# Kernel optimization log

Hardware: AMD Instinct MI355X
Metric: run time of the kernel (lower is better)

Reference implementation:

```python
import jax, jax.numpy as jnp
import numpy as np

NUM_HEADS = 4
LN_EPS = 1e-5


def setup_inputs() -> dict:
    key = jax.random.key(0)
    ks = jax.random.split(key, 12)
    B, S, D = 8, 2048, 256
    Dh = D // NUM_HEADS
    s = 0.02
    return {
        "descriptors": jax.random.normal(ks[0], (B, S, D), jnp.float32),
        # cached rotary embedding (cos, sin) pair broadcastable over heads
        "keypoints": jax.random.normal(ks[1], (2, B, 1, S, Dh), jnp.float32),
        "Wqkv_w": jax.random.normal(ks[2], (3 * D, D), jnp.float32) * s,
        "Wqkv_b": jax.random.normal(ks[3], (3 * D,), jnp.float32) * s,
        "Wo_w": jax.random.normal(ks[4], (D, D), jnp.float32) * s,
        "Wo_b": jax.random.normal(ks[5], (D,), jnp.float32) * s,
        "W1_w": jax.random.normal(ks[6], (2 * D, 2 * D), jnp.float32) * s,
        "W1_b": jax.random.normal(ks[7], (2 * D,), jnp.float32) * s,
        "ln_g": jnp.ones((2 * D,), jnp.float32),
        "ln_b": jnp.zeros((2 * D,), jnp.float32),
        "W2_w": jax.random.normal(ks[8], (D, 2 * D), jnp.float32) * s,
        "W2_b": jax.random.normal(ks[9], (D,), jnp.float32) * s,
    }


def _rotate_half(x):
    # pairwise rotation: (x0,x1,x2,x3,...) -> (-x1,x0,-x3,x2,...)
    xr = x.reshape(x.shape[:-1] + (x.shape[-1] // 2, 2))
    return jnp.stack((-xr[..., 1], xr[..., 0]), axis=-1).reshape(x.shape)


def reference(descriptors, keypoints, Wqkv_w, Wqkv_b, Wo_w, Wo_b,
              W1_w, W1_b, ln_g, ln_b, W2_w, W2_b):
    B, S, D = descriptors.shape
    H = NUM_HEADS
    Dh = D // H
    # fused QKV projection; torch layout: last dim = (H, Dh, 3) interleaved
    qkv = descriptors @ Wqkv_w.T + Wqkv_b           # [B,S,3D]
    qkv = qkv.reshape(B, S, H, Dh, 3).transpose(0, 2, 1, 3, 4)  # [B,H,S,Dh,3]
    q, k, v = qkv[..., 0], qkv[..., 1], qkv[..., 2]
    # rotary embedding on q, k
    cos, sin = keypoints[0], keypoints[1]           # [B,1,S,Dh]
    q = q * cos + _rotate_half(q) * sin
    k = k * cos + _rotate_half(k) * sin
    # scaled dot-product attention
    scale = jnp.float32(Dh) ** -0.5
    sim = jnp.einsum('bhid,bhjd->bhij', q, k) * scale
    attn = jax.nn.softmax(sim, axis=-1)
    ctx = jnp.einsum('bhij,bhjd->bhid', attn, v)    # [B,H,S,Dh]
    ctx = ctx.transpose(0, 2, 1, 3).reshape(B, S, D)
    message = ctx @ Wo_w.T + Wo_b
    # FFN over concat(descriptors, message)
    x = jnp.concatenate([descriptors, message], axis=-1)  # [B,S,2D]
    x = x @ W1_w.T + W1_b
    mu = jnp.mean(x, axis=-1, keepdims=True)
    var = jnp.var(x, axis=-1, keepdims=True)
    x = (x - mu) * jax.lax.rsqrt(var + LN_EPS) * ln_g + ln_b
    x = jax.nn.gelu(x, approximate=False)
    x = x @ W2_w.T + W2_b
    return descriptors + x
```

## Files before the change

kernel.cpp:

```cpp
#include <hip/hip_runtime.h>
#include <math.h>

#define B_  8
#define S_  2048
#define D_  256
#define H_  4
#define DH  64
#define M_  (B_ * S_)
#define QS  4194304

typedef __attribute__((ext_vector_type(8))) short bf16x8;
typedef __attribute__((ext_vector_type(4))) float f32x4;
typedef unsigned short u16;
typedef unsigned int   u32;

#define AS1 __attribute__((address_space(1)))
#define AS3 __attribute__((address_space(3)))

__device__ __forceinline__ u16 f2bf(float x) {
    union { float f; u32 u; } c; c.f = x;
    u32 r = (c.u + 0x7fffu + ((c.u >> 16) & 1u)) >> 16;
    return (u16)r;
}
__device__ __forceinline__ float bf2f(u16 x) {
    union { u32 u; float f; } c; c.u = ((u32)x) << 16;
    return c.f;
}

__device__ __forceinline__ void gload16(const void* g, void* l) {
    __builtin_amdgcn_global_load_lds((const AS1 unsigned int*)g,
                                     (AS3 unsigned int*)l, 16, 0, 0);
}

__global__ __launch_bounds__(256) void cast5_kernel(
    const float* __restrict__ s0, u16* __restrict__ d0,
    const float* __restrict__ s1, u16* __restrict__ d1,
    const float* __restrict__ s2, u16* __restrict__ d2,
    const float* __restrict__ s3, u16* __restrict__ d3,
    const float* __restrict__ s4, u16* __restrict__ d4)
{
    int bid = blockIdx.x;
    const float* s; u16* d;
    if      (bid < 4096) { s = s0; d = d0; }
    else if (bid < 4288) { s = s1; d = d1; bid -= 4096; }
    else if (bid < 4352) { s = s2; d = d2; bid -= 4288; }
    else if (bid < 4608) { s = s3; d = d3; bid -= 4352; }
    else                 { s = s4; d = d4; bid -= 4608; }
    const int i = (bid * 256 + threadIdx.x) * 4;
    const float4 v = *(const float4*)(s + i);
    u16 o[4] = {f2bf(v.x), f2bf(v.y), f2bf(v.z), f2bf(v.w)};
    *(uint2*)(d + i) = *(const uint2*)o;
}

template <int NT, int CONCAT, int RES, int OUTBF16>
__global__ __launch_bounds__(256) void gemm_bf16(
    const u16* __restrict__ A, const u16* __restrict__ A2,
    const u16* __restrict__ W, const float* __restrict__ bias,
    const float* __restrict__ res, float* __restrict__ Cf,
    u16* __restrict__ Cb, int K, int N)
{
    __shared__ u16 As[128 * 64];
    __shared__ u16 Bs[NT * 32 * 64];
    const int tid  = threadIdx.x;
    const int w    = tid >> 6;
    const int lane = tid & 63;
    const int n    = lane & 15;
    const int quad = lane >> 4;
    const int m0   = blockIdx.x * 128;
    const int n0   = blockIdx.y * (NT * 32);
    const int m_off = (w >> 1) * 64;
    const int n_off = (w & 1) * (NT * 16);
    const int lrow = lane >> 3;
    const int lcol = (lane & 7) * 8;

    f32x4 acc[4][NT];
#pragma unroll
    for (int i = 0; i < 4; i++)
#pragma unroll
        for (int j = 0; j < NT; j++) acc[i][j] = (f32x4){0.f, 0.f, 0.f, 0.f};

    for (int k0 = 0; k0 < K; k0 += 64) {
        const u16* Asrc;
        int kb, lda;
        if (CONCAT) { Asrc = (k0 < 256) ? A : A2; kb = k0 & 255; lda = 256; }
        else        { Asrc = A; kb = k0; lda = K; }

        __syncthreads();
#pragma unroll
        for (int it = 0; it < 4; it++) {
            const int r0 = it * 32 + w * 8;
            gload16(Asrc + (size_t)(m0 + r0 + lrow) * lda + kb + lcol, &As[r0 * 64]);
        }
#pragma unroll
        for (int it = 0; it < NT; it++) {
            const int r0 = it * 32 + w * 8;
            gload16(W + (size_t)(n0 + r0 + lrow) * K + k0 + lcol, &Bs[r0 * 64]);
        }
        __syncthreads();

        bf16x8 af[4][2], bf[NT][2];
#pragma unroll
        for (int mt = 0; mt < 4; mt++)
#pragma unroll
            for (int t = 0; t < 2; t++)
                af[mt][t] = *(const bf16x8*)&As[(m_off + mt * 16 + n) * 64 + t * 32 + quad * 8];
#pragma unroll
        for (int nt = 0; nt < NT; nt++)
#pragma unroll
            for (int t = 0; t < 2; t++)
                bf[nt][t] = *(const bf16x8*)&Bs[(n_off + nt * 16 + n) * 64 + t * 32 + quad * 8];

#pragma unroll
        for (int mt = 0; mt < 4; mt++)
#pragma unroll
            for (int nt = 0; nt < NT; nt++) {
                acc[mt][nt] = __builtin_amdgcn_mfma_f32_16x16x32_bf16(af[mt][0], bf[nt][0], acc[mt][nt], 0, 0, 0);
                acc[mt][nt] = __builtin_amdgcn_mfma_f32_16x16x32_bf16(af[mt][1], bf[nt][1], acc[mt][nt], 0, 0, 0);
            }
    }

#pragma unroll
    for (int nt = 0; nt < NT; nt++) {
        const int col = n0 + n_off + nt * 16 + n;
        const float bv = bias[col];
#pragma unroll
        for (int mt = 0; mt < 4; mt++) {
#pragma unroll
            for (int r = 0; r < 4; r++) {
                const int row = m0 + m_off + mt * 16 + quad * 4 + r;
                float o = acc[mt][nt][r] + bv;
                if (RES) o += res[(size_t)row * N + col];
                if (OUTBF16) Cb[(size_t)row * N + col] = f2bf(o);
                else         Cf[(size_t)row * N + col] = o;
            }
        }
    }
}

__global__ __launch_bounds__(256) void rope_kernel(
    const u16* __restrict__ qkv, const float* __restrict__ kp,
    u16* __restrict__ q, u16* __restrict__ k, u16* __restrict__ v)
{
    const int row = blockIdx.x * 2 + (threadIdx.x >> 7);
    const int t   = threadIdx.x & 127;
    const int b   = row >> 11;
    const int s   = row & 2047;
    const int h   = t >> 5;
    const int dp  = t & 31;
    const int d   = dp * 2;

    const u16* src = qkv + (size_t)row * 768 + h * 192 + dp * 6;
    const u32 w0 = *(const u32*)(src);
    const u32 w1 = *(const u32*)(src + 2);
    const u32 w2 = *(const u32*)(src + 4);
    const float qe = bf2f((u16)w0), ke = bf2f((u16)(w0 >> 16));
    const float qo = bf2f((u16)(w1 >> 16));
    const float ko = bf2f((u16)w2);

    const size_t kidx = ((size_t)b * S_ + s) * DH + d;
    const float2 cs = *(const float2*)(kp + kidx);
    const float2 sn = *(const float2*)(kp + (size_t)B_ * S_ * DH + kidx);

    const float qe2 = (qe * cs.x - qo * sn.x) * 0.125f;
    const float qo2 = (qo * cs.y + qe * sn.y) * 0.125f;
    const float ke2 = ke * cs.x - ko * sn.x;
    const float ko2 = ko * cs.y + ke * sn.y;

    const size_t oidx = (((size_t)(b * H_ + h)) * S_ + s) * DH + d;
    *(u32*)(q + oidx) = (u32)f2bf(qe2) | ((u32)f2bf(qo2) << 16);
    *(u32*)(k + oidx) = (u32)f2bf(ke2) | ((u32)f2bf(ko2) << 16);
    *(u32*)(v + oidx) = (w1 & 0xffffu) | (w2 & 0xffff0000u);
}

__global__ __launch_bounds__(256) void vtrans_kernel(
    const u16* __restrict__ v, u16* __restrict__ vt)
{
    const int bh = blockIdx.x;
    const int s  = blockIdx.y * 256 + threadIdx.x;
    const u16* src = v + ((size_t)bh * S_ + s) * DH;
    u16* dst = vt + (size_t)bh * DH * S_ + s;
#pragma unroll
    for (int g = 0; g < 8; g++) {
        const uint4 vv = *(const uint4*)(src + g * 8);
        const u16* us = (const u16*)&vv;
#pragma unroll
        for (int i = 0; i < 8; i++) dst[(size_t)(g * 8 + i) * S_] = us[i];
    }
}

__global__ __launch_bounds__(256, 4) void attn_kernel(
    const u16* __restrict__ q, const u16* __restrict__ k,
    const u16* __restrict__ vt, u16* __restrict__ ctx)
{
    __shared__ u16 ks[128 * 64];
    __shared__ u16 vs[64 * 128];
    __shared__ u16 qs[64 * 64];

    const int tid  = threadIdx.x;
    const int w    = tid >> 6;
    const int lane = tid & 63;
    const int n    = lane & 15;
    const int quad = lane >> 4;
    const int lrow = lane >> 3;
    const int vrow = lane >> 4;
    const int bh   = blockIdx.x;
    const int q0   = blockIdx.y * 64;
    const int b    = bh >> 2;
    const int h    = bh & 3;
    const int nsw  = n & 7;

    const int kcol  = (((lane & 7) ^ lrow) * 8);
    const int vcol0 = (((lane & 15) ^ vrow) * 8);
    const int vcol1 = (((lane & 15) ^ (4 + vrow)) * 8);

    const u16* qbase = q  + (size_t)bh * S_ * DH;
    const u16* kbase = k  + (size_t)bh * S_ * DH;
    const u16* vbase = vt + (size_t)bh * DH * S_;

#pragma unroll
    for (int it = 0; it < 2; it++) {
        const int idx = it * 256 + tid;
        const int row = idx >> 3;
        const int c8  = idx & 7;
        *(uint4*)&qs[row * 64 + ((c8 ^ (row & 7)) * 8)] =
            *(const uint4*)(qbase + (size_t)(q0 + row) * DH + c8 * 8);
    }
    __syncthreads();

    bf16x8 qf[2];
    qf[0] = *(const bf16x8*)&qs[(16 * w + n) * 64 + ((quad       ^ nsw) * 8)];
    qf[1] = *(const bf16x8*)&qs[(16 * w + n) * 64 + (((4 + quad) ^ nsw) * 8)];

    f32x4 o[4];
#pragma unroll
    for (int j = 0; j < 4; j++) o[j] = (f32x4){0.f, 0.f, 0.f, 0.f};
    float lrun[4] = {0.f, 0.f, 0.f, 0.f};

    for (int kb = 0; kb < S_ / 128; kb++) {
        const int k0 = kb * 128;
        __syncthreads();
#pragma unroll
        for (int it = 0; it < 4; it++) {
            const int r0 = w * 32 + it * 8;
            gload16(kbase + (size_t)(k0 + r0 + lrow) * DH + kcol, &ks[r0 * 64]);
            const int d0 = w * 16 + it * 4;
            gload16(vbase + (size_t)(d0 + vrow) * S_ + k0 + ((it & 1) ? vcol1 : vcol0),
                    &vs[d0 * 128]);
        }
        __syncthreads();

        f32x4 sacc[8];
#pragma unroll
        for (int j = 0; j < 8; j++)
            sacc[j] = (f32x4){-12.f, -12.f, -12.f, -12.f};
#pragma unroll
        for (int t = 0; t < 2; t++) {
#pragma unroll
            for (int j = 0; j < 8; j++) {
                const bf16x8 kf = *(const bf16x8*)
                    &ks[(16 * j + n) * 64 + (((t * 4 + quad) ^ nsw) * 8)];
                sacc[j] = __builtin_amdgcn_mfma_f32_16x16x32_bf16(qf[t], kf, sacc[j], 0, 0, 0);
            }
        }
        __syncthreads();

#pragma unroll
        for (int r = 0; r < 4; r++) {
            float rs = 0.f;
            const int rw8  = (quad * 4 + r) & 7;
            const int prow = (16 * w + quad * 4 + r) * 128;
#pragma unroll
            for (int j = 0; j < 8; j++) {
                const float p = __expf(sacc[j][r]);
                rs += p;
                ks[prow + (((2 * j + (n >> 3)) ^ rw8) * 8) + (n & 7)] = f2bf(p);
            }
            lrun[r] += rs;
        }

#pragma unroll
        for (int kt = 0; kt < 4; kt++) {
            const bf16x8 pf = *(const bf16x8*)
                &ks[(16 * w + n) * 128 + (((kt * 4 + quad) ^ nsw) * 8)];
#pragma unroll
            for (int nt = 0; nt < 4; nt++) {
                const bf16x8 vf = *(const bf16x8*)
                    &vs[(16 * nt + n) * 128 + (((kt * 4 + quad) ^ nsw) * 8)];
                o[nt] = __builtin_amdgcn_mfma_f32_16x16x32_bf16(pf, vf, o[nt], 0, 0, 0);
            }
        }
    }

#pragma unroll
    for (int r = 0; r < 4; r++) {
        float s = lrun[r];
        s += __shfl_xor(s, 1);
        s += __shfl_xor(s, 2);
        s += __shfl_xor(s, 4);
        s += __shfl_xor(s, 8);
        lrun[r] = s;
    }

#pragma unroll
    for (int r = 0; r < 4; r++) {
        const float inv = 1.f / lrun[r];
        const int row = q0 + 16 * w + quad * 4 + r;
#pragma unroll
        for (int nt = 0; nt < 4; nt++)
            ctx[((size_t)b * S_ + row) * D_ + h * DH + 16 * nt + n] = f2bf(o[nt][r] * inv);
    }
}

__global__ __launch_bounds__(256) void ln_gelu_kernel(
    const float* __restrict__ x, const float* __restrict__ g,
    const float* __restrict__ bt, u16* __restrict__ y)
{
    __shared__ float ss[4], sqs[4];
    const int m = blockIdx.x;
    const float* row = x + (size_t)m * 512;
    const int t = threadIdx.x;
    const float v0 = row[t];
    const float v1 = row[t + 256];
    float s  = v0 + v1;
    float sq = v0 * v0 + v1 * v1;
#pragma unroll
    for (int off = 1; off < 64; off <<= 1) {
        s  += __shfl_xor(s, off);
        sq += __shfl_xor(sq, off);
    }
    const int w = t >> 6;
    if ((t & 63) == 0) { ss[w] = s; sqs[w] = sq; }
    __syncthreads();
    s  = ss[0] + ss[1] + ss[2] + ss[3];
    sq = sqs[0] + sqs[1] + sqs[2] + sqs[3];
    const float mu   = s * (1.f / 512.f);
    const float var  = sq * (1.f / 512.f) - mu * mu;
    const float rstd = rsqrtf(var + 1e-5f);

    const float y0 = (v0 - mu) * rstd * g[t] + bt[t];
    const float y1 = (v1 - mu) * rstd * g[t + 256] + bt[t + 256];
    y[(size_t)m * 512 + t]       = f2bf(0.5f * y0 * (1.f + erff(y0 * 0.70710678118654752f)));
    y[(size_t)m * 512 + t + 256] = f2bf(0.5f * y1 * (1.f + erff(y1 * 0.70710678118654752f)));
}

extern "C" void kernel_launch(void* const* d_in, const int* in_sizes, int n_in,
                              void* d_out, int out_size, void* d_ws, size_t ws_size,
                              hipStream_t stream)
{
    const float* desc   = (const float*)d_in[0];
    const float* kp     = (const float*)d_in[1];
    const float* Wqkv_w = (const float*)d_in[2];
    const float* Wqkv_b = (const float*)d_in[3];
    const float* Wo_w   = (const float*)d_in[4];
    const float* Wo_b   = (const float*)d_in[5];
    const float* W1_w   = (const float*)d_in[6];
    const float* W1_b   = (const float*)d_in[7];
    const float* ln_g   = (const float*)d_in[8];
    const float* ln_b   = (const float*)d_in[9];
    const float* W2_w   = (const float*)d_in[10];
    const float* W2_b   = (const float*)d_in[11];
    float* out = (float*)d_out;
    float* ws  = (float*)d_ws;

    u16*   qkvb  = (u16*)ws;
    float* x1    = ws;
    u16*   x1b   = (u16*)(ws + 2 * (size_t)QS);
    u16*   qb    = (u16*)(ws + 3 * (size_t)QS);
    u16*   kb    = (u16*)(ws + (size_t)(3.5 * QS));
    u16*   vb    = (u16*)(ws + 4 * (size_t)QS);
    u16*   ctxb  = (u16*)(ws + (size_t)(4.5 * QS));
    u16*   descb = (u16*)(ws + 5 * (size_t)QS);
    u16*   msgb  = (u16*)(ws + (size_t)(5.5 * QS));
    u16*   wpool = (u16*)(ws + 6 * (size_t)QS);
    u16*   vtb   = (u16*)(ws + (size_t)(6.5 * QS));
    u16* wqkvb = wpool;
    u16* wob   = wqkvb + 196608;
    u16* w1b   = wob   + 65536;
    u16* w2b   = w1b   + 262144;

    const dim3 blk(256);

    cast5_kernel<<<dim3(4736), blk, 0, stream>>>(
        desc, descb, Wqkv_w, wqkvb, Wo_w, wob, W1_w, w1b, W2_w, w2b);

    gemm_bf16<4, 0, 0, 1><<<dim3(M_ / 128, 768 / 128), blk, 0, stream>>>(
        descb, nullptr, wqkvb, Wqkv_b, nullptr, nullptr, qkvb, 256, 768);

    rope_kernel<<<dim3(M_ / 2), blk, 0, stream>>>(qkvb, kp, qb, kb, vb);

    vtrans_kernel<<<dim3(B_ * H_, S_ / 256), blk, 0, stream>>>(vb, vtb);

    attn_kernel<<<dim3(B_ * H_, S_ / 64), blk, 0, stream>>>(qb, kb, vtb, ctxb);

    gemm_bf16<2, 0, 0, 1><<<dim3(M_ / 128, 256 / 64), blk, 0, stream>>>(
        ctxb, nullptr, wob, Wo_b, nullptr, nullptr, msgb, 256, 256);

    gemm_bf16<4, 1, 0, 0><<<dim3(M_ / 128, 512 / 128), blk, 0, stream>>>(
        descb, msgb, w1b, W1_b, nullptr, x1, nullptr, 512, 512);

    ln_gelu_kernel<<<dim3(M_), blk, 0, stream>>>(x1, ln_g, ln_b, x1b);

    gemm_bf16<2, 0, 1, 0><<<dim3(M_ / 128, 256 / 64), blk, 0, stream>>>(
        x1b, nullptr, w2b, W2_b, desc, out, nullptr, 512, 256);
}
```

Baseline: 258.4 us.

## Process 128 query rows per attention block to reuse K/V tiles

Each attention workgroup now handles 128 query rows (two 16-row sub-tiles per wave) instead of 64, so every K and V tile loaded into shared memory feeds twice as many MFMAs. The shared-memory buffers are merged into one pool, with the P tile written over the K and Q region. This halves the global K/V traffic and the number of tile-load barriers per query row. In exchange it doubles accumulator registers, drops occupancy from 4 to 2 blocks, and halves the grid to 512 blocks.

```diff
diff --git a/kernel.cpp b/kernel.cpp
--- a/kernel.cpp
+++ b/kernel.cpp
@@ -188,13 +188,14 @@
     }
 }
 
-__global__ __launch_bounds__(256, 4) void attn_kernel(
+__global__ __launch_bounds__(256, 2) void attn_kernel(
     const u16* __restrict__ q, const u16* __restrict__ k,
     const u16* __restrict__ vt, u16* __restrict__ ctx)
 {
-    __shared__ u16 ks[128 * 64];
-    __shared__ u16 vs[64 * 128];
-    __shared__ u16 qs[64 * 64];
+    __shared__ u16 pool[3 * 8192];
+    u16* ks = pool;
+    u16* qs = pool + 8192;
+    u16* vs = pool + 16384;
 
     const int tid  = threadIdx.x;
     const int w    = tid >> 6;
@@ -204,7 +205,7 @@
     const int lrow = lane >> 3;
     const int vrow = lane >> 4;
     const int bh   = blockIdx.x;
-    const int q0   = blockIdx.y * 64;
+    const int q0   = blockIdx.y * 128;
     const int b    = bh >> 2;
     const int h    = bh & 3;
     const int nsw  = n & 7;
@@ -218,7 +219,7 @@
     const u16* vbase = vt + (size_t)bh * DH * S_;
 
 #pragma unroll
-    for (int it = 0; it < 2; it++) {
+    for (int it = 0; it < 4; it++) {
         const int idx = it * 256 + tid;
         const int row = idx >> 3;
         const int c8  = idx & 7;
@@ -227,14 +228,19 @@
     }
     __syncthreads();
 
-    bf16x8 qf[2];
-    qf[0] = *(const bf16x8*)&qs[(16 * w + n) * 64 + ((quad       ^ nsw) * 8)];
-    qf[1] = *(const bf16x8*)&qs[(16 * w + n) * 64 + (((4 + quad) ^ nsw) * 8)];
-
-    f32x4 o[4];
-#pragma unroll
-    for (int j = 0; j < 4; j++) o[j] = (f32x4){0.f, 0.f, 0.f, 0.f};
-    float lrun[4] = {0.f, 0.f, 0.f, 0.f};
+    bf16x8 qf[2][2];
+#pragma unroll
+    for (int mb = 0; mb < 2; mb++) {
+        qf[mb][0] = *(const bf16x8*)&qs[(w * 32 + mb * 16 + n) * 64 + ((quad       ^ nsw) * 8)];
+        qf[mb][1] = *(const bf16x8*)&qs[(w * 32 + mb * 16 + n) * 64 + (((4 + quad) ^ nsw) * 8)];
+    }
+
+    f32x4 o[2][4];
+#pragma unroll
+    for (int mb = 0; mb < 2; mb++)
+#pragma unroll
+        for (int j = 0; j < 4; j++) o[mb][j] = (f32x4){0.f, 0.f, 0.f, 0.f};
+    float lrun[2][4] = {{0.f, 0.f, 0.f, 0.f}, {0.f, 0.f, 0.f, 0.f}};
 
     for (int kb = 0; kb < S_ / 128; kb++) {
         const int k0 = kb * 128;
@@ -249,65 +255,80 @@
         }
         __syncthreads();
 
-        f32x4 sacc[8];
-#pragma unroll
-        for (int j = 0; j < 8; j++)
-            sacc[j] = (f32x4){-12.f, -12.f, -12.f, -12.f};
+        f32x4 sacc[2][8];
+#pragma unroll
+        for (int mb = 0; mb < 2; mb++)
+#pragma unroll
+            for (int j = 0; j < 8; j++)
+                sacc[mb][j] = (f32x4){-12.f, -12.f, -12.f, -12.f};
 #pragma unroll
         for (int t = 0; t < 2; t++) {
 #pragma unroll
             for (int j = 0; j < 8; j++) {
                 const bf16x8 kf = *(const bf16x8*)
                     &ks[(16 * j + n) * 64 + (((t * 4 + quad) ^ nsw) * 8)];
-                sacc[j] = __builtin_amdgcn_mfma_f32_16x16x32_bf16(qf[t], kf, sacc[j], 0, 0, 0);
+                sacc[0][j] = __builtin_amdgcn_mfma_f32_16x16x32_bf16(qf[0][t], kf, sacc[0][j], 0, 0, 0);
+                sacc[1][j] = __builtin_amdgcn_mfma_f32_16x16x32_bf16(qf[1][t], kf, sacc[1][j], 0, 0, 0);
             }
         }
         __syncthreads();
 
 #pragma unroll
-        for (int r = 0; r < 4; r++) {
-            float rs = 0.f;
-            const int rw8  = (quad * 4 + r) & 7;
-            const int prow = (16 * w + quad * 4 + r) * 128;
-#pragma unroll
-            for (int j = 0; j < 8; j++) {
-                const float p = __expf(sacc[j][r]);
-                rs += p;
-                ks[prow + (((2 * j + (n >> 3)) ^ rw8) * 8) + (n & 7)] = f2bf(p);
+        for (int mb = 0; mb < 2; mb++) {
+#pragma unroll
+            for (int r = 0; r < 4; r++) {
+                float rs = 0.f;
+                const int rw8  = (quad * 4 + r) & 7;
+                const int prow = (w * 32 + mb * 16 + quad * 4 + r) * 128;
+#pragma unroll
+                for (int j = 0; j < 8; j++) {
+                    const float p = __expf(sacc[mb][j][r]);
+                    rs += p;
+                    pool[prow + (((2 * j + (n >> 3)) ^ rw8) * 8) + (n & 7)] = f2bf(p);
+                }
+                lrun[mb][r] += rs;
             }
-            lrun[r] += rs;
         }
 
 #pragma unroll
         for (int kt = 0; kt < 4; kt++) {
-            const bf16x8 pf = *(const bf16x8*)
-                &ks[(16 * w + n) * 128 + (((kt * 4 + quad) ^ nsw) * 8)];
+            const bf16x8 pf0 = *(const bf16x8*)
+                &pool[(w * 32 +      n) * 128 + (((kt * 4 + quad) ^ nsw) * 8)];
+            const bf16x8 pf1 = *(const bf16x8*)
+                &pool[(w * 32 + 16 + n) * 128 + (((kt * 4 + quad) ^ nsw) * 8)];
 #pragma unroll
             for (int nt = 0; nt < 4; nt++) {
                 const bf16x8 vf = *(const bf16x8*)
                     &vs[(16 * nt + n) * 128 + (((kt * 4 + quad) ^ nsw) * 8)];
-                o[nt] = __builtin_amdgcn_mfma_f32_16x16x32_bf16(pf, vf, o[nt], 0, 0, 0);
+                o[0][nt] = __builtin_amdgcn_mfma_f32_16x16x32_bf16(pf0, vf, o[0][nt], 0, 0, 0);
+                o[1][nt] = __builtin_amdgcn_mfma_f32_16x16x32_bf16(pf1, vf, o[1][nt], 0, 0, 0);
             }
         }
     }
 
 #pragma unroll
-    for (int r = 0; r < 4; r++) {
-        float s = lrun[r];
-        s += __shfl_xor(s, 1);
-        s += __shfl_xor(s, 2);
-        s += __shfl_xor(s, 4);
-        s += __shfl_xor(s, 8);
-        lrun[r] = s;
-    }
-
-#pragma unroll
-    for (int r = 0; r < 4; r++) {
-        const float inv = 1.f / lrun[r];
-        const int row = q0 + 16 * w + quad * 4 + r;
-#pragma unroll
-        for (int nt = 0; nt < 4; nt++)
-            ctx[((size_t)b * S_ + row) * D_ + h * DH + 16 * nt + n] = f2bf(o[nt][r] * inv);
+    for (int mb = 0; mb < 2; mb++) {
+#pragma unroll
+        for (int r = 0; r < 4; r++) {
+            float s = lrun[mb][r];
+            s += __shfl_xor(s, 1);
+            s += __shfl_xor(s, 2);
+            s += __shfl_xor(s, 4);
+            s += __shfl_xor(s, 8);
+            lrun[mb][r] = s;
+        }
+    }
+
+#pragma unroll
+    for (int mb = 0; mb < 2; mb++) {
+#pragma unroll
+        for (int r = 0; r < 4; r++) {
+            const float inv = 1.f / lrun[mb][r];
+            const int row = q0 + w * 32 + mb * 16 + quad * 4 + r;
+#pragma unroll
+            for (int nt = 0; nt < 4; nt++)
+                ctx[((size_t)b * S_ + row) * D_ + h * DH + 16 * nt + n] = f2bf(o[mb][nt][r] * inv);
+        }
     }
 }
 
@@ -390,7 +411,7 @@
 
     vtrans_kernel<<<dim3(B_ * H_, S_ / 256), blk, 0, stream>>>(vb, vtb);
 
-    attn_kernel<<<dim3(B_ * H_, S_ / 64), blk, 0, stream>>>(qb, kb, vtb, ctxb);
+    attn_kernel<<<dim3(B_ * H_, S_ / 128), blk, 0, stream>>>(qb, kb, vtb, ctxb);
 
     gemm_bf16<2, 0, 0, 1><<<dim3(M_ / 128, 256 / 64), blk, 0, stream>>>(
         ctxb, nullptr, wob, Wo_b, nullptr, nullptr, msgb, 256, 256);
```

Result: faster. 245.5 us (-5.0%).
